# Optimization experiments

Measured on AMD Instinct MI355X. Metric: run time of the kernel, lower is better.

The kernel has to match this reference:

```python
import jax, jax.numpy as jnp
import numpy as np

NUM_HEADS = 16
DEPTH = 0


def rotate_half(x):
    x1, x2 = jnp.split(x, 2, axis=-1)
    return jnp.concatenate((-x2, x1), axis=-1)


def rotary_tables(seq_len, rot_dim, dtype):
    # RotaryEmbedding(dim=rot_dim): inv_freq over even indices of rot_dim
    inv_freq = 1.0 / (10000.0 ** (jnp.arange(0, rot_dim, 2, dtype=jnp.float32) / rot_dim))
    freqs = jnp.arange(seq_len, dtype=jnp.float32)[:, None] * inv_freq[None, :]  # [N, rot_dim/2]
    emb = jnp.concatenate((freqs, freqs), axis=-1)  # [N, rot_dim]
    return emb.astype(dtype), jnp.cos(emb).astype(dtype), jnp.sin(emb).astype(dtype)


def setup_inputs() -> dict:
    key = jax.random.key(0)
    ks = jax.random.split(key, 7)
    B, N, C = 1, 2048, 1024
    hd = C // NUM_HEADS
    std_qkv = (1.0 / C) ** 0.5
    std_proj = (1.0 / (2 * C)) ** 0.5
    return {
        "x": jax.random.normal(ks[0], (B, N, C), dtype=jnp.float32),
        "W_qkv": jax.random.normal(ks[1], (6 * C, C), dtype=jnp.float32) * std_qkv,
        "W_proj": jax.random.normal(ks[2], (C, 2 * C), dtype=jnp.float32) * std_proj,
        "lambda_q1": jax.random.normal(ks[3], (hd,), dtype=jnp.float32) * 0.1,
        "lambda_q2": jax.random.normal(ks[4], (hd,), dtype=jnp.float32) * 0.1,
        "lambda_k1": jax.random.normal(ks[5], (hd,), dtype=jnp.float32) * 0.1,
        "lambda_k2": jax.random.normal(ks[6], (hd,), dtype=jnp.float32) * 0.1,
    }


def reference(x, W_qkv, W_proj, lambda_q1, lambda_q2, lambda_k1, lambda_k2):
    B, N, C = x.shape
    H = NUM_HEADS
    hd = C // H
    scale = hd ** -0.5
    lambda_init = 0.8 - 0.6 * np.exp(-0.3 * DEPTH)

    qkv = jnp.einsum('bnc,dc->bnd', x, W_qkv)               # [B,N,6C]
    qkv = qkv.reshape(B, N, 6, H, hd).transpose(2, 0, 3, 1, 4)  # [6,B,H,N,hd]
    q = jnp.concatenate((qkv[0], qkv[1]), axis=-1)          # [B,H,N,2hd]
    k = jnp.concatenate((qkv[2], qkv[3]), axis=-1)
    v = jnp.concatenate((qkv[4], qkv[5]), axis=-1)

    _, cos, sin = rotary_tables(N, 2 * hd, x.dtype)          # [N,2hd]
    q = q * cos + rotate_half(q) * sin
    k = k * cos + rotate_half(k) * sin

    q1, q2 = jnp.split(q, 2, axis=-1)                        # [B,H,N,hd] each
    k1, k2 = jnp.split(k, 2, axis=-1)

    attn1 = jnp.einsum('bhid,bhjd->bhij', q1, k1) * scale
    attn2 = jnp.einsum('bhid,bhjd->bhij', q2, k2) * scale

    lam1 = jnp.exp(jnp.sum(lambda_q1 * lambda_k1))
    lam2 = jnp.exp(jnp.sum(lambda_q2 * lambda_k2))
    lam = (lam1 - lam2 + lambda_init).astype(x.dtype)

    probs = jax.nn.softmax(attn1, axis=-1) - lam * jax.nn.softmax(attn2, axis=-1)
    out = jnp.einsum('bhij,bhjd->bhid', probs, v)            # [B,H,N,2hd]
    out = out.transpose(0, 2, 1, 3).reshape(B, N, 2 * C)
    out = jnp.einsum('bnd,cd->bnc', out, W_proj)             # [B,N,C]
    return out
```

## Files before the change

kernel.cpp:

```cpp
#include <hip/hip_runtime.h>

using bf16_t = __bf16;
typedef __bf16 bf16x4 __attribute__((ext_vector_type(4)));
typedef __bf16 bf16x8 __attribute__((ext_vector_type(8)));
typedef float floatx4 __attribute__((ext_vector_type(4)));

#define MFMA_BF16(a, b, c) __builtin_amdgcn_mfma_f32_16x16x32_bf16((a), (b), (c), 0, 0, 0)

__device__ __forceinline__ void async_ld16(bf16_t* lds_dst, const bf16_t* g_src) {
    __builtin_amdgcn_global_load_lds(
        (const __attribute__((address_space(1))) void*)g_src,
        (__attribute__((address_space(3))) void*)lds_dst, 16, 0, 0);
}

__global__ __launch_bounds__(256) void cast_bf16(const float* __restrict__ src,
                                                 bf16_t* __restrict__ dst, int n8) {
    int i = blockIdx.x * 256 + threadIdx.x;
    if (i < n8) {
        const floatx4 a = *(const floatx4*)(src + (size_t)i * 8);
        const floatx4 b = *(const floatx4*)(src + (size_t)i * 8 + 4);
        bf16x8 r;
        r[0] = (bf16_t)a[0]; r[1] = (bf16_t)a[1]; r[2] = (bf16_t)a[2]; r[3] = (bf16_t)a[3];
        r[4] = (bf16_t)b[0]; r[5] = (bf16_t)b[1]; r[6] = (bf16_t)b[2]; r[7] = (bf16_t)b[3];
        *(bf16x8*)(dst + (size_t)i * 8) = r;
    }
}

__global__ void lam_kernel(const float* lq1, const float* lq2,
                           const float* lk1, const float* lk2, float* lamp) {
    int l = threadIdx.x;
    float p1 = lq1[l] * lk1[l];
    float p2 = lq2[l] * lk2[l];
    #pragma unroll
    for (int d = 1; d < 64; d <<= 1) {
        p1 += __shfl_xor(p1, d);
        p2 += __shfl_xor(p2, d);
    }
    if (l == 0) *lamp = expf(p1) - expf(p2) + 0.2f;
}

template <int BM, int BN, bool QKV_EPI, typename TC>
__global__ __launch_bounds__(256) void gemm_bt(const bf16_t* __restrict__ A,
                                               const bf16_t* __restrict__ B,
                                               TC* __restrict__ C,
                                               bf16_t* __restrict__ Qb,
                                               bf16_t* __restrict__ Kb,
                                               bf16_t* __restrict__ Vt,
                                               int M, int N, int K) {
    constexpr int BK = 32;
    __shared__ __align__(16) bf16_t As[BM * BK];
    __shared__ __align__(16) bf16_t Bs[BN * BK];
    const int t = threadIdx.x;
    const int lane = t & 63, wave = t >> 6;
    const int q4 = lane >> 4, m16 = lane & 15;
    const int mblk = blockIdx.y * BM, nblk = blockIdx.x * BN;
    const int wr = wave >> 1, wc = wave & 1;
    constexpr int WM = BM / 2, WN = BN / 2;
    constexpr int NI = WM / 16, NJ = WN / 16;
    constexpr int AR = BM * BK / 2048;
    constexpr int BR = BN * BK / 2048;

    floatx4 acc[NI][NJ] = {};

    for (int k0 = 0; k0 < K; k0 += BK) {
        __syncthreads();
        #pragma unroll
        for (int rr = 0; rr < AR; ++rr) {
            int f = rr * 256 + t;
            async_ld16(&As[f * 8], &A[(size_t)(mblk + (f >> 2)) * K + k0 + (f & 3) * 8]);
        }
        #pragma unroll
        for (int rr = 0; rr < BR; ++rr) {
            int f = rr * 256 + t;
            async_ld16(&Bs[f * 8], &B[(size_t)(nblk + (f >> 2)) * K + k0 + (f & 3) * 8]);
        }
        __syncthreads();

        bf16x8 a[NI], b[NJ];
        #pragma unroll
        for (int i = 0; i < NI; ++i)
            a[i] = *(const bf16x8*)&As[(wr * WM + i * 16 + m16) * 32 + q4 * 8];
        #pragma unroll
        for (int j = 0; j < NJ; ++j)
            b[j] = *(const bf16x8*)&Bs[(wc * WN + j * 16 + m16) * 32 + q4 * 8];
        #pragma unroll
        for (int i = 0; i < NI; ++i)
            #pragma unroll
            for (int j = 0; j < NJ; ++j)
                acc[i][j] = MFMA_BF16(a[i], b[j], acc[i][j]);
    }

    #pragma unroll
    for (int i = 0; i < NI; ++i)
        #pragma unroll
        for (int j = 0; j < NJ; ++j) {
            int n = nblk + wc * WN + j * 16 + m16;
            int mbase = mblk + wr * WM + i * 16 + q4 * 4;
            if constexpr (QKV_EPI) {
                int comp = n >> 10, h = (n >> 6) & 15, e = n & 63;
                if (comp < 2) {
                    #pragma unroll
                    for (int r = 0; r < 4; ++r)
                        Qb[(size_t)((comp * 16 + h) * 2048 + mbase + r) * 64 + e] =
                            (bf16_t)acc[i][j][r];
                } else if (comp < 4) {
                    #pragma unroll
                    for (int r = 0; r < 4; ++r)
                        Kb[(size_t)(((comp - 2) * 16 + h) * 2048 + mbase + r) * 64 + e] =
                            (bf16_t)acc[i][j][r];
                } else {
                    bf16x4 pv;
                    #pragma unroll
                    for (int r = 0; r < 4; ++r) pv[r] = (bf16_t)acc[i][j][r];
                    *(bf16x4*)&Vt[(size_t)(h * 128 + (comp - 4) * 64 + e) * 2048 + mbase] = pv;
                }
            } else {
                #pragma unroll
                for (int r = 0; r < 4; ++r)
                    C[(size_t)(mbase + r) * N + n] = (TC)acc[i][j][r];
            }
        }
}

__global__ __launch_bounds__(256) void rotary_inplace(bf16_t* __restrict__ Qb,
                                                      bf16_t* __restrict__ Kb) {
    int t = blockIdx.x * 256 + threadIdx.x;
    int e = t & 63, h = (t >> 6) & 15, n = t >> 10;
    float invf = exp2f(-(float)e * (13.287712379549449f / 64.0f));
    float ang = (float)n * invf;
    float s, c;
    sincosf(ang, &s, &c);
    int off = (h * 2048 + n) * 64 + e;
    float q1 = (float)Qb[off], q2 = (float)Qb[off + 2097152];
    Qb[off]           = (bf16_t)(q1 * c - q2 * s);
    Qb[off + 2097152] = (bf16_t)(q2 * c + q1 * s);
    float k1 = (float)Kb[off], k2 = (float)Kb[off + 2097152];
    Kb[off]           = (bf16_t)(k1 * c - k2 * s);
    Kb[off + 2097152] = (bf16_t)(k2 * c + k1 * s);
}

__global__ __launch_bounds__(512, 4) void flash_diff(const bf16_t* __restrict__ Qb,
                                                     const bf16_t* __restrict__ Kb,
                                                     const bf16_t* __restrict__ Vt,
                                                     const float* __restrict__ lamp,
                                                     bf16_t* __restrict__ Ao) {
    constexpr int N = 2048, BN = 64, NT = N / BN;
    __shared__ __align__(16) bf16_t smem[40960];
    bf16_t* Pf = smem + 32768;
    const int t = threadIdx.x, lane = t & 63, w = t >> 6;
    const int comp = w >> 2, w4 = w & 3;
    const int q4 = lane >> 4, m16 = lane & 15;
    const int Lb = blockIdx.x;
    const int virt = (Lb & 7) * 64 + (Lb >> 3);
    const int h = virt >> 5, qt = virt & 31;
    const float lam = *lamp;
    const float cexp = 0.125f * 1.4426950408889634f;

    bf16x8 qf[2];
    const int qrow = qt * 64 + w4 * 16 + m16;
    #pragma unroll
    for (int kc = 0; kc < 2; ++kc)
        qf[kc] = *(const bf16x8*)&Qb[(size_t)((comp * 16 + h) * 2048 + qrow) * 64 + kc * 32 + q4 * 8];

    bf16x8 ones;
    #pragma unroll
    for (int j = 0; j < 8; ++j) ones[j] = (bf16_t)1.0f;

    floatx4 O[8] = {};
    floatx4 sm = {};

    auto stage = [&](bf16_t* Kd, bf16_t* Vd, int k0) {
        #pragma unroll
        for (int rr = 0; rr < 4; ++rr) {
            int idx = w * 4 + rr;
            if (idx < 16) {
                int i = idx >> 3, s = (idx >> 1) & 3, half = idx & 1;
                async_ld16(&Kd[idx * 512],
                           &Kb[(size_t)((i * 16 + h) * 2048 + k0 + 16 * s + m16) * 64 + half * 32 + q4 * 8]);
            } else {
                int v = idx - 16, tt = v >> 1, half = v & 1;
                async_ld16(&Vd[v * 512],
                           &Vt[(size_t)(h * 128 + tt * 16 + m16) * 2048 + k0 + half * 32 + q4 * 8]);
            }
        }
    };

    stage(smem, smem + 8192, 0);

    for (int it = 0; it < NT; ++it) {
        const int cur = it & 1;
        bf16_t* Kf = smem + cur * 16384;
        bf16_t* Vf = Kf + 8192;
        __syncthreads();
        if (it + 1 < NT) {
            bf16_t* Kn = smem + (cur ^ 1) * 16384;
            stage(Kn, Kn + 8192, (it + 1) * BN);
        }

        bf16_t* pw = &Pf[w * 1024];
        __builtin_amdgcn_s_setprio(1);
        #pragma unroll
        for (int s = 0; s < 4; ++s) {
            floatx4 sacc = {};
            const bf16x8 kf0 = *(const bf16x8*)&Kf[((comp * 4 + s) * 2 + 0) * 512 + lane * 8];
            const bf16x8 kf1 = *(const bf16x8*)&Kf[((comp * 4 + s) * 2 + 1) * 512 + lane * 8];
            sacc = MFMA_BF16(qf[0], kf0, sacc);
            sacc = MFMA_BF16(qf[1], kf1, sacc);
            __builtin_amdgcn_s_setprio(0);
            const int half = s >> 1, quad = (2 * s + (m16 >> 3)) & 3, jj = m16 & 7;
            #pragma unroll
            for (int r = 0; r < 4; ++r) {
                int u = quad * 16 + q4 * 4 + r;
                pw[half * 512 + (u ^ quad) * 8 + jj] = (bf16_t)exp2f(sacc[r] * cexp);
            }
            __builtin_amdgcn_s_setprio(1);
        }

        bf16x8 pf[2];
        const int ur = lane ^ q4;
        pf[0] = *(const bf16x8*)&pw[0 * 512 + ur * 8];
        pf[1] = *(const bf16x8*)&pw[1 * 512 + ur * 8];
        sm = MFMA_BF16(pf[0], ones, sm);
        sm = MFMA_BF16(pf[1], ones, sm);
        #pragma unroll
        for (int tt = 0; tt < 8; ++tt) {
            const bf16x8 vf0 = *(const bf16x8*)&Vf[(tt * 2 + 0) * 512 + lane * 8];
            const bf16x8 vf1 = *(const bf16x8*)&Vf[(tt * 2 + 1) * 512 + lane * 8];
            O[tt] = MFMA_BF16(pf[0], vf0, O[tt]);
            O[tt] = MFMA_BF16(pf[1], vf1, O[tt]);
        }
        __builtin_amdgcn_s_setprio(0);
    }

    float inv[4];
    #pragma unroll
    for (int r = 0; r < 4; ++r) inv[r] = 1.0f / sm[r];

    float* Ff = (float*)smem;
    __syncthreads();
    if (comp == 1) {
        #pragma unroll
        for (int tt = 0; tt < 8; ++tt) {
            floatx4 val;
            #pragma unroll
            for (int r = 0; r < 4; ++r) val[r] = lam * O[tt][r] * inv[r];
            *(floatx4*)&Ff[((w4 * 128 + tt * 16 + m16) << 4) + q4 * 4] = val;
        }
    }
    __syncthreads();
    if (comp == 0) {
        const int orow = qt * 64 + w4 * 16 + q4 * 4;
        #pragma unroll
        for (int tt = 0; tt < 8; ++tt) {
            const floatx4 v1 = *(const floatx4*)&Ff[((w4 * 128 + tt * 16 + m16) << 4) + q4 * 4];
            #pragma unroll
            for (int r = 0; r < 4; ++r) {
                float val = O[tt][r] * inv[r] - v1[r];
                Ao[(size_t)(orow + r) * 2048 + h * 128 + tt * 16 + m16] = (bf16_t)val;
            }
        }
    }
}

extern "C" void kernel_launch(void* const* d_in, const int* in_sizes, int n_in,
                              void* d_out, int out_size, void* d_ws, size_t ws_size,
                              hipStream_t stream) {
    const float* x     = (const float*)d_in[0];
    const float* Wqkv  = (const float*)d_in[1];
    const float* Wproj = (const float*)d_in[2];
    const float* lq1   = (const float*)d_in[3];
    const float* lq2   = (const float*)d_in[4];
    const float* lk1   = (const float*)d_in[5];
    const float* lk2   = (const float*)d_in[6];
    float* out = (float*)d_out;

    char* ws = (char*)d_ws;
    bf16_t* xb     = (bf16_t*)(ws);
    bf16_t* Ao     = (bf16_t*)(ws);
    bf16_t* Wqkvb  = (bf16_t*)(ws + 4194304);
    bf16_t* Wprojb = (bf16_t*)(ws + 16777216);
    bf16_t* Qb     = (bf16_t*)(ws + 20971520);
    bf16_t* Kb     = (bf16_t*)(ws + 29360128);
    bf16_t* Vt     = (bf16_t*)(ws + 37748736);
    float*  lamp   = (float*)(ws + 46137344);

    lam_kernel<<<1, 64, 0, stream>>>(lq1, lq2, lk1, lk2, lamp);
    cast_bf16<<<1024, 256, 0, stream>>>(x, xb, 2048 * 1024 / 8);
    cast_bf16<<<3072, 256, 0, stream>>>(Wqkv, Wqkvb, 6144 * 1024 / 8);
    cast_bf16<<<1024, 256, 0, stream>>>(Wproj, Wprojb, 1024 * 2048 / 8);
    gemm_bt<128, 128, true, float><<<dim3(48, 16), 256, 0, stream>>>(
        xb, Wqkvb, (float*)nullptr, Qb, Kb, Vt, 2048, 6144, 1024);
    rotary_inplace<<<(2048 * 16 * 64) / 256, 256, 0, stream>>>(Qb, Kb);
    flash_diff<<<512, 512, 0, stream>>>(Qb, Kb, Vt, lamp, Ao);
    gemm_bt<128, 64, false, float><<<dim3(16, 16), 256, 0, stream>>>(
        Ao, Wprojb, out, (bf16_t*)nullptr, (bf16_t*)nullptr, (bf16_t*)nullptr,
        2048, 1024, 2048);
}
```

Before: 253.3 us.

## Restructure diff-attention work split: per-wave K slices, direct K loads, 2x4 PV tiles

Reassigns work inside the flash_diff block so each wave computes scores for one 16-key slice against all 64 queries, loading K straight from global into registers with a one-tile prefetch instead of staging K through LDS. P tiles are shared in LDS and each wave then computes a 32x64 output tile, reusing P and V fragments across two MFMA chains. Row sums are accumulated in registers and reduced with shuffles and LDS, which replaces the ones-matrix MFMA. This cuts LDS footprint and the per-wave V reads, at the cost of an extra barrier per iteration and uncoalesced-ish global K loads.

```diff
diff --git a/kernel.cpp b/kernel.cpp
--- a/kernel.cpp
+++ b/kernel.cpp
@@ -145,10 +145,10 @@
                                                      const float* __restrict__ lamp,
                                                      bf16_t* __restrict__ Ao) {
     constexpr int N = 2048, BN = 64, NT = N / BN;
-    __shared__ __align__(16) bf16_t smem[40960];
-    bf16_t* Pf = smem + 32768;
+    __shared__ __align__(16) bf16_t smem[24576];
+    bf16_t* Pf = smem + 16384;
     const int t = threadIdx.x, lane = t & 63, w = t >> 6;
-    const int comp = w >> 2, w4 = w & 3;
+    const int comp = w >> 2, sub = w & 3;
     const int q4 = lane >> 4, m16 = lane & 15;
     const int Lb = blockIdx.x;
     const int virt = (Lb & 7) * 64 + (Lb >> 3);
@@ -156,109 +156,137 @@
     const float lam = *lamp;
     const float cexp = 0.125f * 1.4426950408889634f;
 
-    bf16x8 qf[2];
-    const int qrow = qt * 64 + w4 * 16 + m16;
+    const int kq = sub;
+    const int aa = sub >> 1, bb = sub & 1;
+
+    bf16x8 qf[4][2];
     #pragma unroll
-    for (int kc = 0; kc < 2; ++kc)
-        qf[kc] = *(const bf16x8*)&Qb[(size_t)((comp * 16 + h) * 2048 + qrow) * 64 + kc * 32 + q4 * 8];
-
-    bf16x8 ones;
+    for (int qq = 0; qq < 4; ++qq)
+        #pragma unroll
+        for (int e = 0; e < 2; ++e)
+            qf[qq][e] = *(const bf16x8*)&Qb[(size_t)((comp * 16 + h) * 2048 +
+                             qt * 64 + qq * 16 + m16) * 64 + e * 32 + q4 * 8];
+
+    const bf16_t* kbase = &Kb[(size_t)((comp * 16 + h) * 2048 + 16 * kq + m16) * 64 + q4 * 8];
+    bf16x8 kcur0 = *(const bf16x8*)(kbase);
+    bf16x8 kcur1 = *(const bf16x8*)(kbase + 32);
+    bf16x8 knext0, knext1;
+
+    const int uhi = 2 * (kq & 1) + (q4 >> 1);
+    const int poff = (uhi * 16 + (m16 ^ uhi)) * 8 + (q4 & 1) * 4;
+    const int kc_w = kq >> 1;
+
+    auto stageV = [&](bf16_t* Vd, int k0) {
+        #pragma unroll
+        for (int rr = 0; rr < 2; ++rr) {
+            int idx = w * 2 + rr;
+            int tt = idx >> 1, half = idx & 1;
+            async_ld16(&Vd[idx * 512],
+                       &Vt[(size_t)(h * 128 + tt * 16 + m16) * 2048 + k0 + half * 32 + q4 * 8]);
+        }
+    };
+    stageV(smem, 0);
+
+    floatx4 O[2][4] = {};
+    float rs[4] = {};
+
+    #pragma unroll 2
+    for (int it = 0; it < NT; ++it) {
+        bf16_t* Vb = smem + (it & 1) * 8192;
+        __syncthreads();
+
+        if (it + 1 < NT) {
+            const bf16_t* kb = kbase + (size_t)(it + 1) * 4096;
+            knext0 = *(const bf16x8*)(kb);
+            knext1 = *(const bf16x8*)(kb + 32);
+        }
+
+        __builtin_amdgcn_s_setprio(1);
+        #pragma unroll
+        for (int qq = 0; qq < 4; ++qq) {
+            floatx4 s = {};
+            s = MFMA_BF16(kcur0, qf[qq][0], s);
+            s = MFMA_BF16(kcur1, qf[qq][1], s);
+            __builtin_amdgcn_s_setprio(0);
+            float p0 = exp2f(s[0] * cexp), p1 = exp2f(s[1] * cexp);
+            float p2 = exp2f(s[2] * cexp), p3 = exp2f(s[3] * cexp);
+            rs[qq] += (p0 + p1) + (p2 + p3);
+            bf16x4 wv;
+            wv[0] = (bf16_t)p0; wv[1] = (bf16_t)p1; wv[2] = (bf16_t)p2; wv[3] = (bf16_t)p3;
+            *(bf16x4*)&Pf[((comp * 4 + qq) * 2 + kc_w) * 512 + poff] = wv;
+            __builtin_amdgcn_s_setprio(1);
+        }
+        __builtin_amdgcn_s_setprio(0);
+        __syncthreads();
+
+        if (it + 1 < NT) stageV(smem + (((it & 1) ^ 1) * 8192), (it + 1) * BN);
+
+        const int ur = (lane ^ q4) * 8;
+        bf16x8 pf00 = *(const bf16x8*)&Pf[((comp * 4 + 2 * aa + 0) * 2 + 0) * 512 + ur];
+        bf16x8 pf01 = *(const bf16x8*)&Pf[((comp * 4 + 2 * aa + 0) * 2 + 1) * 512 + ur];
+        bf16x8 pf10 = *(const bf16x8*)&Pf[((comp * 4 + 2 * aa + 1) * 2 + 0) * 512 + ur];
+        bf16x8 pf11 = *(const bf16x8*)&Pf[((comp * 4 + 2 * aa + 1) * 2 + 1) * 512 + ur];
+        __builtin_amdgcn_s_setprio(1);
+        #pragma unroll
+        for (int vv = 0; vv < 4; ++vv) {
+            const bf16x8 vf0 = *(const bf16x8*)&Vb[((bb * 4 + vv) * 2 + 0) * 512 + lane * 8];
+            const bf16x8 vf1 = *(const bf16x8*)&Vb[((bb * 4 + vv) * 2 + 1) * 512 + lane * 8];
+            O[0][vv] = MFMA_BF16(pf00, vf0, O[0][vv]);
+            O[0][vv] = MFMA_BF16(pf01, vf1, O[0][vv]);
+            O[1][vv] = MFMA_BF16(pf10, vf0, O[1][vv]);
+            O[1][vv] = MFMA_BF16(pf11, vf1, O[1][vv]);
+        }
+        __builtin_amdgcn_s_setprio(0);
+        kcur0 = knext0;
+        kcur1 = knext1;
+    }
+
     #pragma unroll
-    for (int j = 0; j < 8; ++j) ones[j] = (bf16_t)1.0f;
-
-    floatx4 O[8] = {};
-    floatx4 sm = {};
-
-    auto stage = [&](bf16_t* Kd, bf16_t* Vd, int k0) {
-        #pragma unroll
-        for (int rr = 0; rr < 4; ++rr) {
-            int idx = w * 4 + rr;
-            if (idx < 16) {
-                int i = idx >> 3, s = (idx >> 1) & 3, half = idx & 1;
-                async_ld16(&Kd[idx * 512],
-                           &Kb[(size_t)((i * 16 + h) * 2048 + k0 + 16 * s + m16) * 64 + half * 32 + q4 * 8]);
-            } else {
-                int v = idx - 16, tt = v >> 1, half = v & 1;
-                async_ld16(&Vd[v * 512],
-                           &Vt[(size_t)(h * 128 + tt * 16 + m16) * 2048 + k0 + half * 32 + q4 * 8]);
-            }
-        }
-    };
-
-    stage(smem, smem + 8192, 0);
-
-    for (int it = 0; it < NT; ++it) {
-        const int cur = it & 1;
-        bf16_t* Kf = smem + cur * 16384;
-        bf16_t* Vf = Kf + 8192;
-        __syncthreads();
-        if (it + 1 < NT) {
-            bf16_t* Kn = smem + (cur ^ 1) * 16384;
-            stage(Kn, Kn + 8192, (it + 1) * BN);
-        }
-
-        bf16_t* pw = &Pf[w * 1024];
-        __builtin_amdgcn_s_setprio(1);
-        #pragma unroll
-        for (int s = 0; s < 4; ++s) {
-            floatx4 sacc = {};
-            const bf16x8 kf0 = *(const bf16x8*)&Kf[((comp * 4 + s) * 2 + 0) * 512 + lane * 8];
-            const bf16x8 kf1 = *(const bf16x8*)&Kf[((comp * 4 + s) * 2 + 1) * 512 + lane * 8];
-            sacc = MFMA_BF16(qf[0], kf0, sacc);
-            sacc = MFMA_BF16(qf[1], kf1, sacc);
-            __builtin_amdgcn_s_setprio(0);
-            const int half = s >> 1, quad = (2 * s + (m16 >> 3)) & 3, jj = m16 & 7;
+    for (int qq = 0; qq < 4; ++qq) {
+        rs[qq] += __shfl_xor(rs[qq], 16);
+        rs[qq] += __shfl_xor(rs[qq], 32);
+    }
+    __syncthreads();
+    float* Rs = (float*)Pf;
+    if (q4 == 0) {
+        #pragma unroll
+        for (int qq = 0; qq < 4; ++qq)
+            Rs[((comp * 4 + qq) * 16 + m16) * 4 + kq] = rs[qq];
+    }
+    float* Ff = (float*)smem;
+    if (comp == 1) {
+        #pragma unroll
+        for (int i = 0; i < 2; ++i)
+            #pragma unroll
+            for (int vv = 0; vv < 4; ++vv)
+                *(floatx4*)&Ff[(aa * 2 + bb) * 2048 + ((i * 4 + vv) * 16 + m16) * 16 + q4 * 4] =
+                    O[i][vv];
+    }
+    __syncthreads();
+    if (comp == 0) {
+        float inv0[2][4], inv1l[2][4];
+        #pragma unroll
+        for (int i = 0; i < 2; ++i)
             #pragma unroll
             for (int r = 0; r < 4; ++r) {
-                int u = quad * 16 + q4 * 4 + r;
-                pw[half * 512 + (u ^ quad) * 8 + jj] = (bf16_t)exp2f(sacc[r] * cexp);
+                const floatx4 s0 = *(const floatx4*)&Rs[((2 * aa + i) * 16 + q4 * 4 + r) * 4];
+                const floatx4 s1 = *(const floatx4*)&Rs[((4 + 2 * aa + i) * 16 + q4 * 4 + r) * 4];
+                inv0[i][r] = 1.0f / ((s0[0] + s0[1]) + (s0[2] + s0[3]));
+                inv1l[i][r] = lam / ((s1[0] + s1[1]) + (s1[2] + s1[3]));
             }
-            __builtin_amdgcn_s_setprio(1);
-        }
-
-        bf16x8 pf[2];
-        const int ur = lane ^ q4;
-        pf[0] = *(const bf16x8*)&pw[0 * 512 + ur * 8];
-        pf[1] = *(const bf16x8*)&pw[1 * 512 + ur * 8];
-        sm = MFMA_BF16(pf[0], ones, sm);
-        sm = MFMA_BF16(pf[1], ones, sm);
-        #pragma unroll
-        for (int tt = 0; tt < 8; ++tt) {
-            const bf16x8 vf0 = *(const bf16x8*)&Vf[(tt * 2 + 0) * 512 + lane * 8];
-            const bf16x8 vf1 = *(const bf16x8*)&Vf[(tt * 2 + 1) * 512 + lane * 8];
-            O[tt] = MFMA_BF16(pf[0], vf0, O[tt]);
-            O[tt] = MFMA_BF16(pf[1], vf1, O[tt]);
-        }
-        __builtin_amdgcn_s_setprio(0);
-    }
-
-    float inv[4];
-    #pragma unroll
-    for (int r = 0; r < 4; ++r) inv[r] = 1.0f / sm[r];
-
-    float* Ff = (float*)smem;
-    __syncthreads();
-    if (comp == 1) {
-        #pragma unroll
-        for (int tt = 0; tt < 8; ++tt) {
-            floatx4 val;
+        #pragma unroll
+        for (int i = 0; i < 2; ++i)
             #pragma unroll
-            for (int r = 0; r < 4; ++r) val[r] = lam * O[tt][r] * inv[r];
-            *(floatx4*)&Ff[((w4 * 128 + tt * 16 + m16) << 4) + q4 * 4] = val;
-        }
-    }
-    __syncthreads();
-    if (comp == 0) {
-        const int orow = qt * 64 + w4 * 16 + q4 * 4;
-        #pragma unroll
-        for (int tt = 0; tt < 8; ++tt) {
-            const floatx4 v1 = *(const floatx4*)&Ff[((w4 * 128 + tt * 16 + m16) << 4) + q4 * 4];
-            #pragma unroll
-            for (int r = 0; r < 4; ++r) {
-                float val = O[tt][r] * inv[r] - v1[r];
-                Ao[(size_t)(orow + r) * 2048 + h * 128 + tt * 16 + m16] = (bf16_t)val;
+            for (int vv = 0; vv < 4; ++vv) {
+                const floatx4 o1 = *(const floatx4*)&Ff[(aa * 2 + bb) * 2048 +
+                                       ((i * 4 + vv) * 16 + m16) * 16 + q4 * 4];
+                #pragma unroll
+                for (int r = 0; r < 4; ++r) {
+                    float val = O[i][vv][r] * inv0[i][r] - o1[r] * inv1l[i][r];
+                    Ao[(size_t)(qt * 64 + (2 * aa + i) * 16 + q4 * 4 + r) * 2048 +
+                       h * 128 + (bb * 4 + vv) * 16 + m16] = (bf16_t)val;
+                }
             }
-        }
     }
 }
 
```

Result: slower. 279.7 us (+10.4%).

## Load K fragments directly into registers and stage only V through LDS

Applied to the files above, without the earlier changes.

Each wave now loads its K fragments straight from global memory into registers, prefetching the next tile during the current one. Only V is staged asynchronously through a smaller double buffer in LDS. This cuts LDS use and LDS reads for K and could let more blocks fit per CU. The cost is more registers and possibly uncoalesced or redundant global K loads, since each comp group loads K itself.

```diff
diff --git a/kernel.cpp b/kernel.cpp
--- a/kernel.cpp
+++ b/kernel.cpp
@@ -145,8 +145,8 @@
                                                      const float* __restrict__ lamp,
                                                      bf16_t* __restrict__ Ao) {
     constexpr int N = 2048, BN = 64, NT = N / BN;
-    __shared__ __align__(16) bf16_t smem[40960];
-    bf16_t* Pf = smem + 32768;
+    __shared__ __align__(16) bf16_t smem[24576];
+    bf16_t* Pf = smem + 16384;
     const int t = threadIdx.x, lane = t & 63, w = t >> 6;
     const int comp = w >> 2, w4 = w & 3;
     const int q4 = lane >> 4, m16 = lane & 15;
@@ -169,43 +169,36 @@
     floatx4 O[8] = {};
     floatx4 sm = {};
 
-    auto stage = [&](bf16_t* Kd, bf16_t* Vd, int k0) {
-        #pragma unroll
-        for (int rr = 0; rr < 4; ++rr) {
-            int idx = w * 4 + rr;
-            if (idx < 16) {
-                int i = idx >> 3, s = (idx >> 1) & 3, half = idx & 1;
-                async_ld16(&Kd[idx * 512],
-                           &Kb[(size_t)((i * 16 + h) * 2048 + k0 + 16 * s + m16) * 64 + half * 32 + q4 * 8]);
-            } else {
-                int v = idx - 16, tt = v >> 1, half = v & 1;
-                async_ld16(&Vd[v * 512],
-                           &Vt[(size_t)(h * 128 + tt * 16 + m16) * 2048 + k0 + half * 32 + q4 * 8]);
-            }
+    const bf16_t* kroot = &Kb[(size_t)((comp * 16 + h) * 2048 + m16) * 64 + q4 * 8];
+    bf16x8 kf[4][2];
+    #pragma unroll
+    for (int s = 0; s < 4; ++s) {
+        kf[s][0] = *(const bf16x8*)(kroot + s * 1024);
+        kf[s][1] = *(const bf16x8*)(kroot + s * 1024 + 32);
+    }
+
+    auto stageV = [&](bf16_t* Vd, int k0) {
+        #pragma unroll
+        for (int rr = 0; rr < 2; ++rr) {
+            int idx = w * 2 + rr;
+            int tt = idx >> 1, half = idx & 1;
+            async_ld16(&Vd[idx * 512],
+                       &Vt[(size_t)(h * 128 + tt * 16 + m16) * 2048 + k0 + half * 32 + q4 * 8]);
         }
     };
-
-    stage(smem, smem + 8192, 0);
+    stageV(smem, 0);
 
     for (int it = 0; it < NT; ++it) {
-        const int cur = it & 1;
-        bf16_t* Kf = smem + cur * 16384;
-        bf16_t* Vf = Kf + 8192;
+        bf16_t* Vb = smem + (it & 1) * 8192;
         __syncthreads();
-        if (it + 1 < NT) {
-            bf16_t* Kn = smem + (cur ^ 1) * 16384;
-            stage(Kn, Kn + 8192, (it + 1) * BN);
-        }
 
         bf16_t* pw = &Pf[w * 1024];
         __builtin_amdgcn_s_setprio(1);
         #pragma unroll
         for (int s = 0; s < 4; ++s) {
             floatx4 sacc = {};
-            const bf16x8 kf0 = *(const bf16x8*)&Kf[((comp * 4 + s) * 2 + 0) * 512 + lane * 8];
-            const bf16x8 kf1 = *(const bf16x8*)&Kf[((comp * 4 + s) * 2 + 1) * 512 + lane * 8];
-            sacc = MFMA_BF16(qf[0], kf0, sacc);
-            sacc = MFMA_BF16(qf[1], kf1, sacc);
+            sacc = MFMA_BF16(qf[0], kf[s][0], sacc);
+            sacc = MFMA_BF16(qf[1], kf[s][1], sacc);
             __builtin_amdgcn_s_setprio(0);
             const int half = s >> 1, quad = (2 * s + (m16 >> 3)) & 3, jj = m16 & 7;
             #pragma unroll
@@ -214,6 +207,17 @@
                 pw[half * 512 + (u ^ quad) * 8 + jj] = (bf16_t)exp2f(sacc[r] * cexp);
             }
             __builtin_amdgcn_s_setprio(1);
+        }
+        __builtin_amdgcn_s_setprio(0);
+
+        if (it + 1 < NT) {
+            const bf16_t* kb = kroot + (size_t)(it + 1) * 4096;
+            #pragma unroll
+            for (int s = 0; s < 4; ++s) {
+                kf[s][0] = *(const bf16x8*)(kb + s * 1024);
+                kf[s][1] = *(const bf16x8*)(kb + s * 1024 + 32);
+            }
+            stageV(smem + (((it & 1) ^ 1) * 8192), (it + 1) * BN);
         }
 
         bf16x8 pf[2];
@@ -222,10 +226,11 @@
         pf[1] = *(const bf16x8*)&pw[1 * 512 + ur * 8];
         sm = MFMA_BF16(pf[0], ones, sm);
         sm = MFMA_BF16(pf[1], ones, sm);
+        __builtin_amdgcn_s_setprio(1);
         #pragma unroll
         for (int tt = 0; tt < 8; ++tt) {
-            const bf16x8 vf0 = *(const bf16x8*)&Vf[(tt * 2 + 0) * 512 + lane * 8];
-            const bf16x8 vf1 = *(const bf16x8*)&Vf[(tt * 2 + 1) * 512 + lane * 8];
+            const bf16x8 vf0 = *(const bf16x8*)&Vb[(tt * 2 + 0) * 512 + lane * 8];
+            const bf16x8 vf1 = *(const bf16x8*)&Vb[(tt * 2 + 1) * 512 + lane * 8];
             O[tt] = MFMA_BF16(pf[0], vf0, O[tt]);
             O[tt] = MFMA_BF16(pf[1], vf1, O[tt]);
         }
```

Result: slower. 323.5 us (+27.7%).
